# Kernel tuning notes

Hardware: AMD Instinct MI355X
Metric: run time of the kernel (lower is better)

## Reference

```python
import jax, jax.numpy as jnp
import numpy as np

LAMBDA_SOFTMAX = 9.0  # opt.lambda_softmax (smooth)
LAMBDA_LSE = 6.0      # opt.lambda_lse (LogSumExp aggregation)
EPS = 1e-8


def l2norm(x, axis, eps=EPS):
    # matches torch l2norm: x / (sqrt(sum(x^2)) + eps)
    return x / (jnp.sqrt(jnp.sum(x * x, axis=axis, keepdims=True)) + eps)


def setup_inputs() -> dict:
    key = jax.random.key(0)
    k1, k2 = jax.random.split(key)
    images = jax.random.normal(k1, (128, 36, 256), dtype=jnp.float32)    # (n_image, n_regions, d)
    captions = jax.random.normal(k2, (256, 48, 256), dtype=jnp.float32)  # (n_caption, max_n_word, d)
    return {"images": images, "captions": captions}


def reference(images, captions):
    """Vectorized SCAN xattn_score_t2i with raw_feature_norm='clipped_l2norm',
    agg_func='LogSumExp'. Returns (n_image, n_caption) similarity matrix.
    Axes: c=caption, i=image, r=region (sourceL), w=word (queryL), d=embed."""
    # func_attention: attn = bmm(context, query^T) -> (b, sourceL, queryL); here batched over (c, i)
    attn = jnp.einsum('ird,cwd->cirw', images, captions)       # [c,i,r,w]
    # first norm: LeakyReLU(0.1) then l2norm over queryL dim (torch dim=2 of (b,r,w))
    attn = jax.nn.leaky_relu(attn, negative_slope=0.1)
    attn = l2norm(attn, axis=3)
    # transpose to (b, queryL, sourceL) and smoothed softmax over sourceL
    attn = jnp.swapaxes(attn, 2, 3)                            # [c,i,w,r]
    attn = jax.nn.softmax(attn * LAMBDA_SOFTMAX, axis=-1)
    # weightedContext = attn @ context  -> (b, queryL, d)
    wctx = jnp.einsum('ciwr,ird->ciwd', attn, images)          # [c,i,w,d]
    # cosine similarity over d between expanded caption words and weighted context
    cap = captions[:, None, :, :]                              # [c,1,w,d]
    w12 = jnp.sum(cap * wctx, axis=-1)                         # [c,i,w]
    w1 = jnp.sqrt(jnp.sum(cap * cap, axis=-1))
    w2 = jnp.sqrt(jnp.sum(wctx * wctx, axis=-1))
    row_sim = w12 / jnp.maximum(w1 * w2, EPS)                  # [c,i,w]
    # LogSumExp aggregation over words: log(sum exp(s*lse)) / lse
    sim = jax.scipy.special.logsumexp(row_sim * LAMBDA_LSE, axis=-1) / LAMBDA_LSE  # [c,i]
    return sim.T                                               # (n_image, n_caption)
```

## Files before the change

kernel.cpp:

```cpp
#include <hip/hip_runtime.h>
#include <math.h>

#define NI 128
#define NC 256
#define NR 36
#define NW 48
#define ND 256

#define PIB 264
#define PG  72
#define PSP 40

#define SOFT_SCALE 12.984255368000671f

typedef __bf16 bf16;
typedef __bf16 bf16x8 __attribute__((ext_vector_type(8)));
typedef __bf16 bf16x4 __attribute__((ext_vector_type(4)));
typedef float  f32x4  __attribute__((ext_vector_type(4)));

#define OFF_IB    0
#define OFF_G     25344
#define OFF_P     32256
#define OFF_GUARD 47616
#define SMEM_TOTAL 47744

#define MFMA16(A,B,C) __builtin_amdgcn_mfma_f32_16x16x32_bf16(A, B, C, 0, 0, 0)

__device__ __forceinline__ float dpp_add16(float v) {
    int x = __builtin_bit_cast(int, v);
    v += __builtin_bit_cast(float, __builtin_amdgcn_update_dpp(0, x, 0xB1, 0xF, 0xF, true));
    x = __builtin_bit_cast(int, v);
    v += __builtin_bit_cast(float, __builtin_amdgcn_update_dpp(0, x, 0x4E, 0xF, 0xF, true));
    x = __builtin_bit_cast(int, v);
    v += __builtin_bit_cast(float, __builtin_amdgcn_update_dpp(0, x, 0x141, 0xF, 0xF, true));
    x = __builtin_bit_cast(int, v);
    v += __builtin_bit_cast(float, __builtin_amdgcn_update_dpp(0, x, 0x140, 0xF, 0xF, true));
    return v;
}

__device__ __forceinline__ float lrelu(float t) { return t > 0.f ? t : 0.1f * t; }

__global__ __launch_bounds__(256)
void prep_kernel(const float* __restrict__ captions, bf16* __restrict__ capb,
                 float* __restrict__ w1g)
{
    const int c = blockIdx.x >> 2, q = blockIdx.x & 3;
    const int wave = threadIdx.x >> 6, lane = threadIdx.x & 63;
    #pragma unroll
    for (int j = 0; j < 3; ++j) {
        int w = q * 12 + wave * 3 + j;
        size_t off = ((size_t)c * NW + w) * ND + lane * 4;
        float4 v = *(const float4*)(captions + off);
        bf16x4 h = { (bf16)v.x, (bf16)v.y, (bf16)v.z, (bf16)v.w };
        *(bf16x4*)(capb + off) = h;
        float s = v.x*v.x + v.y*v.y + v.z*v.z + v.w*v.w;
        s += __shfl_xor(s, 1);  s += __shfl_xor(s, 2);  s += __shfl_xor(s, 4);
        s += __shfl_xor(s, 8);  s += __shfl_xor(s, 16); s += __shfl_xor(s, 32);
        if (lane == 0) w1g[c * NW + w] = sqrtf(s);
    }
}

__device__ __forceinline__ bf16x8 ld_cvt_f32(const float* p, float& ss) {
    float4 lo = *(const float4*)p;
    float4 hi = *(const float4*)(p + 4);
    ss += lo.x*lo.x + lo.y*lo.y + lo.z*lo.z + lo.w*lo.w
        + hi.x*hi.x + hi.y*hi.y + hi.z*hi.z + hi.w*hi.w;
    bf16x8 r = { (bf16)lo.x, (bf16)lo.y, (bf16)lo.z, (bf16)lo.w,
                 (bf16)hi.x, (bf16)hi.y, (bf16)hi.z, (bf16)hi.w };
    return r;
}

template<bool USE_WS>
__global__ __launch_bounds__(256, 3)
void scan_main(const float* __restrict__ images,
               const float* __restrict__ captions,
               const bf16* __restrict__ capb,
               const float* __restrict__ w1g,
               float* __restrict__ out)
{
    __shared__ __align__(16) unsigned char smem[SMEM_TOTAL];
    bf16* sIb = (bf16*)(smem + OFF_IB);
    bf16* sG  = (bf16*)(smem + OFF_G);

    const int tid  = threadIdx.x;
    const int wave = tid >> 6;
    const int lane = tid & 63;
    const int quad = lane >> 4;
    const int l15  = lane & 15;
    const int i    = blockIdx.x >> 3;
    const int c0   = (blockIdx.x & 7) * 32;

    bf16* sPw = (bf16*)(smem + OFF_P) + wave * (48 * PSP);

    const float* gI = images + (size_t)i * NR * ND;
    #pragma unroll
    for (int k = 0; k < 9; ++k) {
        int t = tid + k * 256;
        int e = t * 4, r = e >> 8, d = e & 255;
        float4 v = *(const float4*)(gI + e);
        bf16x4 h = { (bf16)v.x, (bf16)v.y, (bf16)v.z, (bf16)v.w };
        *(bf16x4*)&sIb[r * PIB + d] = h;
    }
    {
        uint32_t* pIb = (uint32_t*)sIb;
        #pragma unroll
        for (int k = 0; k < 7; ++k) { int x = tid + k * 256; if (x < 1584) pIb[4752 + x] = 0u; }
        uint32_t* pG = (uint32_t*)sG;
        #pragma unroll
        for (int k = 0; k < 7; ++k) { int x = tid + k * 256; if (x < 1728) pG[x] = 0u; }
        uint32_t* pP = (uint32_t*)(smem + OFF_P);
        #pragma unroll
        for (int k = 0; k < 16; ++k) { int x = tid + k * 256; if (x < 3872) pP[x] = 0u; }
    }
    __syncthreads();

    if (wave < 3) {
        f32x4 g0 = {0,0,0,0}, g1 = {0,0,0,0}, g2 = {0,0,0,0};
        #pragma unroll
        for (int ks = 0; ks < 8; ++ks) {
            bf16x8 a  = *(const bf16x8*)&sIb[(wave * 16 + l15) * PIB + ks * 32 + quad * 8];
            bf16x8 b0 = *(const bf16x8*)&sIb[(l15)      * PIB + ks * 32 + quad * 8];
            bf16x8 b1 = *(const bf16x8*)&sIb[(16 + l15) * PIB + ks * 32 + quad * 8];
            bf16x8 b2 = *(const bf16x8*)&sIb[(32 + l15) * PIB + ks * 32 + quad * 8];
            g0 = MFMA16(a, b0, g0); g1 = MFMA16(a, b1, g1); g2 = MFMA16(a, b2, g2);
        }
        #pragma unroll
        for (int p = 0; p < 4; ++p) {
            int m = wave * 16 + quad * 4 + p;
            sG[m * PG + l15]      = (bf16)g0[p];
            sG[m * PG + 16 + l15] = (bf16)g1[p];
            sG[m * PG + 32 + l15] = (bf16)g2[p];
        }
    }
    __syncthreads();

    bf16x8 bg0[3], bg1[3];
    #pragma unroll
    for (int nt = 0; nt < 3; ++nt) {
        bg0[nt] = *(const bf16x8*)&sG[(nt * 16 + l15) * PG + quad * 8];
        bg1[nt] = *(const bf16x8*)&sG[(nt * 16 + l15) * PG + 32 + quad * 8];
    }

    for (int it = 0; it < 8; ++it) {
        const int c = c0 + wave * 8 + it;

        float w1v[3][4];
        if (USE_WS) {
            #pragma unroll
            for (int mt = 0; mt < 3; ++mt)
                #pragma unroll
                for (int p = 0; p < 4; ++p)
                    w1v[mt][p] = w1g[(size_t)c * NW + mt * 16 + quad * 4 + p];
        }

        f32x4 acc[3][3] = {};
        float ssc[3] = {0.f, 0.f, 0.f};
        const bf16*  ab   = USE_WS ? capb + ((size_t)c * NW + l15) * ND + quad * 8 : nullptr;
        const float* ab32 = USE_WS ? nullptr : captions + ((size_t)c * NW + l15) * ND + quad * 8;
        #pragma unroll
        for (int ks = 0; ks < 8; ++ks) {
            bf16x8 a0, a1, a2;
            if (USE_WS) {
                a0 = *(const bf16x8*)(ab + ks * 32);
                a1 = *(const bf16x8*)(ab + 16 * ND + ks * 32);
                a2 = *(const bf16x8*)(ab + 32 * ND + ks * 32);
            } else {
                a0 = ld_cvt_f32(ab32 + ks * 32, ssc[0]);
                a1 = ld_cvt_f32(ab32 + 16 * ND + ks * 32, ssc[1]);
                a2 = ld_cvt_f32(ab32 + 32 * ND + ks * 32, ssc[2]);
            }
            bf16x8 b0 = *(const bf16x8*)&sIb[(l15)      * PIB + ks * 32 + quad * 8];
            bf16x8 b1 = *(const bf16x8*)&sIb[(16 + l15) * PIB + ks * 32 + quad * 8];
            bf16x8 b2 = *(const bf16x8*)&sIb[(32 + l15) * PIB + ks * 32 + quad * 8];
            acc[0][0] = MFMA16(a0, b0, acc[0][0]);
            acc[1][0] = MFMA16(a1, b0, acc[1][0]);
            acc[2][0] = MFMA16(a2, b0, acc[2][0]);
            acc[0][1] = MFMA16(a0, b1, acc[0][1]);
            acc[1][1] = MFMA16(a1, b1, acc[1][1]);
            acc[2][1] = MFMA16(a2, b1, acc[2][1]);
            acc[0][2] = MFMA16(a0, b2, acc[0][2]);
            acc[1][2] = MFMA16(a1, b2, acc[1][2]);
            acc[2][2] = MFMA16(a2, b2, acc[2][2]);
        }
        if (!USE_WS) {
            #pragma unroll
            for (int mt = 0; mt < 3; ++mt) {
                float s = ssc[mt];
                s += __shfl_xor(s, 16); s += __shfl_xor(s, 32);
                ssc[mt] = sqrtf(s);
            }
            #pragma unroll
            for (int mt = 0; mt < 3; ++mt)
                #pragma unroll
                for (int p = 0; p < 4; ++p)
                    w1v[mt][p] = __shfl(ssc[mt], (lane & 48) + quad * 4 + p);
        }

        float inv[3];
        #pragma unroll
        for (int nt = 0; nt < 3; ++nt) {
            float s = 0.f;
            #pragma unroll
            for (int mt = 0; mt < 3; ++mt)
                #pragma unroll
                for (int p = 0; p < 4; ++p) { float t = lrelu(acc[mt][nt][p]); s += t * t; }
            s += __shfl_xor(s, 16); s += __shfl_xor(s, 32);
            inv[nt] = SOFT_SCALE / (sqrtf(s) + 1e-8f);
        }

        float q[3][3][4];
        float w12v[3][4];
        #pragma unroll
        for (int mt = 0; mt < 3; ++mt) {
            #pragma unroll
            for (int p = 0; p < 4; ++p) {
                float e0 = exp2f(lrelu(acc[mt][0][p]) * inv[0]);
                float e1 = exp2f(lrelu(acc[mt][1][p]) * inv[1]);
                float e2 = (l15 < 4) ? exp2f(lrelu(acc[mt][2][p]) * inv[2]) : 0.f;
                w12v[mt][p] = dpp_add16(e0 * acc[mt][0][p] + e1 * acc[mt][1][p]
                                       + e2 * acc[mt][2][p]);
                q[mt][0][p] = e0; q[mt][1][p] = e1; q[mt][2][p] = e2;
                int row = mt * 16 + quad * 4 + p;
                sPw[row * PSP + l15]      = (bf16)e0;
                sPw[row * PSP + 16 + l15] = (bf16)e1;
                if (l15 < 4) sPw[row * PSP + 32 + l15] = (bf16)e2;
            }
        }

        f32x4 pg[3][3] = {};
        #pragma unroll
        for (int mt = 0; mt < 3; ++mt) {
            const bf16* ap = &sPw[(mt * 16 + l15) * PSP];
            bf16x8 pa0 = *(const bf16x8*)(ap + quad * 8);
            bf16x8 pa1 = *(const bf16x8*)(ap + 32 + quad * 8);
            #pragma unroll
            for (int nt = 0; nt < 3; ++nt) {
                pg[mt][nt] = MFMA16(pa0, bg0[nt], pg[mt][nt]);
                pg[mt][nt] = MFMA16(pa1, bg1[nt], pg[mt][nt]);
            }
        }

        float esum = 0.f;
        #pragma unroll
        for (int mt = 0; mt < 3; ++mt) {
            #pragma unroll
            for (int p = 0; p < 4; ++p) {
                float s2 = pg[mt][0][p] * q[mt][0][p]
                         + pg[mt][1][p] * q[mt][1][p]
                         + pg[mt][2][p] * q[mt][2][p];
                s2 = dpp_add16(s2);
                float w2v = sqrtf(fmaxf(s2, 0.f));
                float rsim = w12v[mt][p] / fmaxf(w1v[mt][p] * w2v, 1e-8f);
                esum += __expf(6.0f * rsim);
            }
        }
        esum += __shfl_xor(esum, 16); esum += __shfl_xor(esum, 32);
        if (lane == 0) out[(size_t)i * NC + c] = logf(esum) * (1.0f / 6.0f);
    }
}

extern "C" void kernel_launch(void* const* d_in, const int* in_sizes, int n_in,
                              void* d_out, int out_size, void* d_ws, size_t ws_size,
                              hipStream_t stream) {
    const float* images   = (const float*)d_in[0];
    const float* captions = (const float*)d_in[1];
    float* out = (float*)d_out;

    const size_t need_w1  = (size_t)NC * NW * sizeof(float);
    const size_t need_cap = (size_t)NC * NW * ND * 2;
    bool use_ws = ws_size >= need_w1 + need_cap;

    dim3 grid(1024), block(256);
    if (use_ws) {
        float* w1g = (float*)d_ws;
        bf16*  capb = (bf16*)((char*)d_ws + need_w1);
        hipLaunchKernelGGL(prep_kernel, dim3(1024), dim3(256), 0, stream, captions, capb, w1g);
        hipLaunchKernelGGL((scan_main<true>), grid, block, 0, stream, images, captions, capb, w1g, out);
    } else {
        hipLaunchKernelGGL((scan_main<false>), grid, block, 0, stream, images, captions,
                           (const bf16*)nullptr, (const float*)nullptr, out);
    }
}
```

Baseline: 187.3 us.

## Use overlapping region tile to shrink LDS and interleave softmax with Gram MFMA

The third region tile now starts at row 20 instead of 32, overlapping rows 20-31, so the image tile no longer needs zero-padded rows and the Gram matrix is stored at a narrower pitch. Lanes only use the last four columns of that tile, and the padding zero-fill is dropped, which cuts shared memory enough to raise launch bounds to four blocks per CU. The per-mt softmax, P@G MFMA and similarity reduction are fused into one loop so the q and pg arrays no longer stay live across all row tiles, lowering register pressure. The overlapped indexing is delicate and risks correctness if any masked column or row mapping is off, and it adds more LDS traffic per CU at higher occupancy.

```diff
diff --git a/kernel.cpp b/kernel.cpp
--- a/kernel.cpp
+++ b/kernel.cpp
@@ -8,7 +8,7 @@
 #define ND 256
 
 #define PIB 264
-#define PG  72
+#define PG  64
 #define PSP 40
 
 #define SOFT_SCALE 12.984255368000671f
@@ -19,10 +19,10 @@
 typedef float  f32x4  __attribute__((ext_vector_type(4)));
 
 #define OFF_IB    0
-#define OFF_G     25344
-#define OFF_P     32256
-#define OFF_GUARD 47616
-#define SMEM_TOTAL 47744
+#define OFF_G     19008
+#define OFF_P     23616
+#define OFF_GUARD 38976
+#define SMEM_TOTAL 39104
 
 #define MFMA16(A,B,C) __builtin_amdgcn_mfma_f32_16x16x32_bf16(A, B, C, 0, 0, 0)
 
@@ -71,7 +71,7 @@
 }
 
 template<bool USE_WS>
-__global__ __launch_bounds__(256, 3)
+__global__ __launch_bounds__(256, 4)
 void scan_main(const float* __restrict__ images,
                const float* __restrict__ captions,
                const bf16* __restrict__ capb,
@@ -92,6 +92,8 @@
 
     bf16* sPw = (bf16*)(smem + OFF_P) + wave * (48 * PSP);
 
+    const int rb2 = 20;
+
     const float* gI = images + (size_t)i * NR * ND;
     #pragma unroll
     for (int k = 0; k < 9; ++k) {
@@ -102,34 +104,32 @@
         *(bf16x4*)&sIb[r * PIB + d] = h;
     }
     {
-        uint32_t* pIb = (uint32_t*)sIb;
-        #pragma unroll
-        for (int k = 0; k < 7; ++k) { int x = tid + k * 256; if (x < 1584) pIb[4752 + x] = 0u; }
         uint32_t* pG = (uint32_t*)sG;
         #pragma unroll
-        for (int k = 0; k < 7; ++k) { int x = tid + k * 256; if (x < 1728) pG[x] = 0u; }
+        for (int k = 0; k < 5; ++k) { int x = tid + k * 256; if (x < 1152) pG[x] = 0u; }
         uint32_t* pP = (uint32_t*)(smem + OFF_P);
         #pragma unroll
-        for (int k = 0; k < 16; ++k) { int x = tid + k * 256; if (x < 3872) pP[x] = 0u; }
+        for (int k = 0; k < 16; ++k) { int x = tid + k * 256; if (x < 3904) pP[x] = 0u; }
     }
     __syncthreads();
 
     if (wave < 3) {
+        const int mb = (wave == 2) ? rb2 : wave * 16;
         f32x4 g0 = {0,0,0,0}, g1 = {0,0,0,0}, g2 = {0,0,0,0};
         #pragma unroll
         for (int ks = 0; ks < 8; ++ks) {
-            bf16x8 a  = *(const bf16x8*)&sIb[(wave * 16 + l15) * PIB + ks * 32 + quad * 8];
-            bf16x8 b0 = *(const bf16x8*)&sIb[(l15)      * PIB + ks * 32 + quad * 8];
-            bf16x8 b1 = *(const bf16x8*)&sIb[(16 + l15) * PIB + ks * 32 + quad * 8];
-            bf16x8 b2 = *(const bf16x8*)&sIb[(32 + l15) * PIB + ks * 32 + quad * 8];
+            bf16x8 a  = *(const bf16x8*)&sIb[(mb + l15)  * PIB + ks * 32 + quad * 8];
+            bf16x8 b0 = *(const bf16x8*)&sIb[(l15)       * PIB + ks * 32 + quad * 8];
+            bf16x8 b1 = *(const bf16x8*)&sIb[(16 + l15)  * PIB + ks * 32 + quad * 8];
+            bf16x8 b2 = *(const bf16x8*)&sIb[(rb2 + l15) * PIB + ks * 32 + quad * 8];
             g0 = MFMA16(a, b0, g0); g1 = MFMA16(a, b1, g1); g2 = MFMA16(a, b2, g2);
         }
         #pragma unroll
         for (int p = 0; p < 4; ++p) {
-            int m = wave * 16 + quad * 4 + p;
-            sG[m * PG + l15]      = (bf16)g0[p];
-            sG[m * PG + 16 + l15] = (bf16)g1[p];
-            sG[m * PG + 32 + l15] = (bf16)g2[p];
+            int m = mb + quad * 4 + p;
+            sG[m * PG + l15]       = (bf16)g0[p];
+            sG[m * PG + 16 + l15]  = (bf16)g1[p];
+            sG[m * PG + rb2 + l15] = (bf16)g2[p];
         }
     }
     __syncthreads();
@@ -137,8 +137,9 @@
     bf16x8 bg0[3], bg1[3];
     #pragma unroll
     for (int nt = 0; nt < 3; ++nt) {
-        bg0[nt] = *(const bf16x8*)&sG[(nt * 16 + l15) * PG + quad * 8];
-        bg1[nt] = *(const bf16x8*)&sG[(nt * 16 + l15) * PG + 32 + quad * 8];
+        int rbn = (nt == 2) ? rb2 : nt * 16;
+        bg0[nt] = *(const bf16x8*)&sG[(rbn + l15) * PG + quad * 8];
+        bg1[nt] = *(const bf16x8*)&sG[(rbn + l15) * PG + 32 + quad * 8];
     }
 
     for (int it = 0; it < 8; ++it) {
@@ -169,9 +170,9 @@
                 a1 = ld_cvt_f32(ab32 + 16 * ND + ks * 32, ssc[1]);
                 a2 = ld_cvt_f32(ab32 + 32 * ND + ks * 32, ssc[2]);
             }
-            bf16x8 b0 = *(const bf16x8*)&sIb[(l15)      * PIB + ks * 32 + quad * 8];
-            bf16x8 b1 = *(const bf16x8*)&sIb[(16 + l15) * PIB + ks * 32 + quad * 8];
-            bf16x8 b2 = *(const bf16x8*)&sIb[(32 + l15) * PIB + ks * 32 + quad * 8];
+            bf16x8 b0 = *(const bf16x8*)&sIb[(l15)       * PIB + ks * 32 + quad * 8];
+            bf16x8 b1 = *(const bf16x8*)&sIb[(16 + l15)  * PIB + ks * 32 + quad * 8];
+            bf16x8 b2 = *(const bf16x8*)&sIb[(rb2 + l15) * PIB + ks * 32 + quad * 8];
             acc[0][0] = MFMA16(a0, b0, acc[0][0]);
             acc[1][0] = MFMA16(a1, b0, acc[1][0]);
             acc[2][0] = MFMA16(a2, b0, acc[2][0]);
@@ -208,49 +209,36 @@
             inv[nt] = SOFT_SCALE / (sqrtf(s) + 1e-8f);
         }
 
-        float q[3][3][4];
-        float w12v[3][4];
+        float esum = 0.f;
         #pragma unroll
         for (int mt = 0; mt < 3; ++mt) {
+            float q0[4], q1[4], q2[4], w12v[4];
             #pragma unroll
             for (int p = 0; p < 4; ++p) {
                 float e0 = exp2f(lrelu(acc[mt][0][p]) * inv[0]);
                 float e1 = exp2f(lrelu(acc[mt][1][p]) * inv[1]);
-                float e2 = (l15 < 4) ? exp2f(lrelu(acc[mt][2][p]) * inv[2]) : 0.f;
-                w12v[mt][p] = dpp_add16(e0 * acc[mt][0][p] + e1 * acc[mt][1][p]
-                                       + e2 * acc[mt][2][p]);
-                q[mt][0][p] = e0; q[mt][1][p] = e1; q[mt][2][p] = e2;
+                float e2 = (l15 >= 12) ? exp2f(lrelu(acc[mt][2][p]) * inv[2]) : 0.f;
+                w12v[p] = dpp_add16(e0 * acc[mt][0][p] + e1 * acc[mt][1][p]
+                                   + e2 * acc[mt][2][p]);
+                q0[p] = e0; q1[p] = e1; q2[p] = e2;
                 int row = mt * 16 + quad * 4 + p;
                 sPw[row * PSP + l15]      = (bf16)e0;
                 sPw[row * PSP + 16 + l15] = (bf16)e1;
-                if (l15 < 4) sPw[row * PSP + 32 + l15] = (bf16)e2;
-            }
-        }
-
-        f32x4 pg[3][3] = {};
-        #pragma unroll
-        for (int mt = 0; mt < 3; ++mt) {
+                if (l15 >= 12) sPw[row * PSP + rb2 + l15] = (bf16)e2;
+            }
             const bf16* ap = &sPw[(mt * 16 + l15) * PSP];
             bf16x8 pa0 = *(const bf16x8*)(ap + quad * 8);
             bf16x8 pa1 = *(const bf16x8*)(ap + 32 + quad * 8);
-            #pragma unroll
-            for (int nt = 0; nt < 3; ++nt) {
-                pg[mt][nt] = MFMA16(pa0, bg0[nt], pg[mt][nt]);
-                pg[mt][nt] = MFMA16(pa1, bg1[nt], pg[mt][nt]);
-            }
-        }
-
-        float esum = 0.f;
-        #pragma unroll
-        for (int mt = 0; mt < 3; ++mt) {
+            f32x4 pg0 = {0,0,0,0}, pg1 = {0,0,0,0}, pg2 = {0,0,0,0};
+            pg0 = MFMA16(pa0, bg0[0], pg0); pg0 = MFMA16(pa1, bg1[0], pg0);
+            pg1 = MFMA16(pa0, bg0[1], pg1); pg1 = MFMA16(pa1, bg1[1], pg1);
+            pg2 = MFMA16(pa0, bg0[2], pg2); pg2 = MFMA16(pa1, bg1[2], pg2);
             #pragma unroll
             for (int p = 0; p < 4; ++p) {
-                float s2 = pg[mt][0][p] * q[mt][0][p]
-                         + pg[mt][1][p] * q[mt][1][p]
-                         + pg[mt][2][p] * q[mt][2][p];
+                float s2 = pg0[p] * q0[p] + pg1[p] * q1[p] + pg2[p] * q2[p];
                 s2 = dpp_add16(s2);
                 float w2v = sqrtf(fmaxf(s2, 0.f));
-                float rsim = w12v[mt][p] / fmaxf(w1v[mt][p] * w2v, 1e-8f);
+                float rsim = w12v[p] / fmaxf(w1v[mt][p] * w2v, 1e-8f);
                 esum += __expf(6.0f * rsim);
             }
         }
```

Result: slower. 218.7 us (+16.8%).
